# Optimization experiments

Measured on AMD Instinct MI355X. Metric: run time of the kernel, lower is better.

Reference implementation:

```python
import jax, jax.numpy as jnp
import numpy as np

T, D, E, F = 8192, 1024, 8, 3584


def setup_inputs() -> dict:
    key = jax.random.key(0)
    ks = jax.random.split(key, 5)
    scale_in = 1.0 / np.sqrt(D)
    scale_ff = 1.0 / np.sqrt(F)
    return {
        "x": jax.random.normal(ks[0], (T, D), dtype=jnp.float32),
        "w1": jax.random.normal(ks[1], (E, F, D), dtype=jnp.float32) * scale_in,
        "w3": jax.random.normal(ks[2], (E, F, D), dtype=jnp.float32) * scale_in,
        "w2": jax.random.normal(ks[3], (E, D, F), dtype=jnp.float32) * scale_ff,
        "router_logits": jax.random.normal(ks[4], (T, E), dtype=jnp.float32),
        "top_k": 2,
    }


def reference(x, w1, w3, w2, router_logits, top_k):
    # Routing: softmax over experts, keep top-k, renormalize (Mixtral, normalize=True)
    probs = jax.nn.softmax(router_logits, axis=-1)            # [T, E]
    top_vals, top_idx = jax.lax.top_k(probs, top_k)           # [T, k]
    top_vals = top_vals / jnp.sum(top_vals, axis=-1, keepdims=True)
    tokens = jnp.arange(x.shape[0])[:, None]
    weights = jnp.zeros_like(probs).at[tokens, top_idx].set(top_vals)  # [T, E]

    gate = jnp.einsum('td,efd->tef', x, w1)                   # [T, E, F]
    up = jnp.einsum('td,efd->tef', x, w3)                     # [T, E, F]
    h = jax.nn.silu(gate) * up                                # [T, E, F]
    out = jnp.einsum('te,tef,edf->td', weights, h, w2)        # [T, D]
    return out
```

## Files before the change

kernel.cpp:

```cpp
#include <hip/hip_runtime.h>
#include <cstdint>

#define T_TOK 8192
#define D_DIM 1024
#define E_EXP 8
#define F_DIM 3584
#define NROW  (2 * T_TOK)
#define PROWS_PAD 18432
#define MAXTILES 72
#define MAXBANDS 18
#define G1_GRID (MAXBANDS * 112)
#define W2_ELEMS ((long)E_EXP * D_DIM * F_DIM)
#define W2_CVT_BLOCKS ((int)(W2_ELEMS / (512 * 8)))
#define W13_ELEMS ((long)E_EXP * F_DIM * D_DIM)
#define GATH_BLOCKS (PROWS_PAD * 128 / 256)
#define W13_BLOCKS ((int)(W13_ELEMS / 8 / 256))

typedef __attribute__((ext_vector_type(8))) __bf16 bf16x8;
typedef __attribute__((ext_vector_type(4))) float f32x4;

__device__ __forceinline__ void gload16(const void* g, void* l) {
    __builtin_amdgcn_global_load_lds(
        (const __attribute__((address_space(1))) void*)(g),
        (__attribute__((address_space(3))) void*)(l),
        16, 0, 0);
}

__device__ __forceinline__ void cvt8(const float* __restrict__ in, __bf16* __restrict__ out, long i) {
    const float4 f0 = *(const float4*)(in + i);
    const float4 f1 = *(const float4*)(in + i + 4);
    bf16x8 o;
    o[0] = (__bf16)f0.x; o[1] = (__bf16)f0.y; o[2] = (__bf16)f0.z; o[3] = (__bf16)f0.w;
    o[4] = (__bf16)f1.x; o[5] = (__bf16)f1.y; o[6] = (__bf16)f1.z; o[7] = (__bf16)f1.w;
    *(bf16x8*)(out + i) = o;
}

__global__ void cvt_kernel(const float* __restrict__ in, __bf16* __restrict__ out, long n) {
    long i = ((long)blockIdx.x * blockDim.x + threadIdx.x) * 8;
    if (i >= n) return;
    cvt8(in, out, i);
}

__global__ void prep_kernel(const float* __restrict__ x, const int* __restrict__ tokOf,
                            __bf16* __restrict__ xg,
                            const float* __restrict__ w1, __bf16* __restrict__ w1b,
                            const float* __restrict__ w3, __bf16* __restrict__ w3b) {
    const int b = blockIdx.x;
    if (b < GATH_BLOCKS) {
        const int idx = b * 256 + threadIdx.x;
        const int pr = idx >> 7;
        const int j = (idx & 127) * 8;
        const int tk = tokOf[pr];
        bf16x8 o = {};
        if (tk >= 0) {
            const float4 f0 = *(const float4*)(x + (long)tk * D_DIM + j);
            const float4 f1 = *(const float4*)(x + (long)tk * D_DIM + j + 4);
            o[0] = (__bf16)f0.x; o[1] = (__bf16)f0.y; o[2] = (__bf16)f0.z; o[3] = (__bf16)f0.w;
            o[4] = (__bf16)f1.x; o[5] = (__bf16)f1.y; o[6] = (__bf16)f1.z; o[7] = (__bf16)f1.w;
        }
        *(bf16x8*)(xg + (long)pr * D_DIM + j) = o;
    } else if (b < GATH_BLOCKS + W13_BLOCKS) {
        const long i = ((long)(b - GATH_BLOCKS) * 256 + threadIdx.x) * 8;
        if (i < W13_ELEMS) cvt8(w1, w1b, i);
    } else {
        const long i = ((long)(b - GATH_BLOCKS - W13_BLOCKS) * 256 + threadIdx.x) * 8;
        if (i < W13_ELEMS) cvt8(w3, w3b, i);
    }
}

__global__ void route_kernel(const float* __restrict__ rl, int* cnt,
                             int* __restrict__ eidx, float* __restrict__ ewgt) {
    int t = blockIdx.x * blockDim.x + threadIdx.x;
    if (t >= T_TOK) return;
    float l[8];
#pragma unroll
    for (int e = 0; e < 8; ++e) l[e] = rl[t * 8 + e];
    int i0 = 0; float v0 = l[0];
    int i1 = -1; float v1 = -1e30f;
#pragma unroll
    for (int e = 1; e < 8; ++e) {
        if (l[e] > v0) { v1 = v0; i1 = i0; v0 = l[e]; i0 = e; }
        else if (l[e] > v1) { v1 = l[e]; i1 = e; }
    }
    float wsec = 1.f / (1.f + __expf(v0 - v1));
    eidx[2 * t] = i0; eidx[2 * t + 1] = i1;
    ewgt[2 * t] = 1.f - wsec; ewgt[2 * t + 1] = wsec;
    atomicAdd(&cnt[i0], 1); atomicAdd(&cnt[i1], 1);
}

__global__ void scan_kernel(const int* __restrict__ cnt, int* __restrict__ pofs) {
    if (threadIdx.x == 0) {
        int a = 0;
        for (int e = 0; e < E_EXP; ++e) { pofs[e] = a; a += (cnt[e] + 255) & ~255; }
        pofs[E_EXP] = a;
    }
}

__global__ void tiles_kernel(const int* __restrict__ pofs, int* __restrict__ tile_e,
                             int* __restrict__ tile_r0, int* __restrict__ meta) {
    if (threadIdx.x == 0) {
        int n = 0;
        for (int e = 0; e < E_EXP; ++e)
            for (int r = pofs[e]; r < pofs[e + 1]; r += 256) {
                tile_e[n] = e; tile_r0[n] = r; ++n;
            }
        meta[0] = n;
    }
}

__global__ void assign_kernel(const int* __restrict__ eidx, const int* __restrict__ pofs,
                              int* cnt2, int* __restrict__ tokOf, int* __restrict__ rowOf) {
    int t = blockIdx.x * blockDim.x + threadIdx.x;
    if (t >= T_TOK) return;
#pragma unroll
    for (int s = 0; s < 2; ++s) {
        int e = eidx[2 * t + s];
        int pos = atomicAdd(&cnt2[e], 1);
        int prow = pofs[e] + pos;
        tokOf[prow] = t;
        rowOf[2 * t + s] = prow;
    }
}

__device__ __forceinline__ int chunk_row(int c) { return ((c >> 7) << 4) | ((c >> 2) & 15); }
__device__ __forceinline__ int chunk_col(int c) {
    return ((c >> 6) & 1) * 32 + (((c & 3) * 8) ^ (((c >> 5) & 1) << 4));
}

template <int NT>
__device__ __forceinline__ void moe_pipeline(
    const __bf16* const (&srcA)[2][2], const __bf16* const (&srcB)[2][2],
    __bf16 (&Ash)[2][2][8192], __bf16 (&Bsh)[2][2][8192],
    int wave, int abase, int wm, int bh, int bsel, f32x4 (&acc)[8][4])
{
    auto stA = [&](int buf, int kt, int h) {
        const long k0 = (long)kt * 64;
        gload16(srcA[h][0] + k0, &Ash[buf][h][(0 * 512 + wave * 64) * 8]);
        gload16(srcA[h][1] + k0, &Ash[buf][h][(1 * 512 + wave * 64) * 8]);
    };
    auto stB = [&](int buf, int kt, int h) {
        const long k0 = (long)kt * 64;
        gload16(srcB[h][0] + k0, &Bsh[buf][h][(0 * 512 + wave * 64) * 8]);
        gload16(srcB[h][1] + k0, &Bsh[buf][h][(1 * 512 + wave * 64) * 8]);
    };

    bf16x8 bfr[4][2];
    bf16x8 afr[4][2];
    bf16x8 afr2[4][2];

#define LD_A4(dst, Ab, h) \
    _Pragma("unroll") for (int j = 0; j < 4; ++j) { \
        dst[j][0] = *(const bf16x8*)((Ab) + ((4*(h)+j) * 2 + 0) * 512); \
        dst[j][1] = *(const bf16x8*)((Ab) + ((4*(h)+j) * 2 + 1) * 512); \
    }

#define LD_B(Bb) \
    _Pragma("unroll") for (int ni = 0; ni < 4; ++ni) { \
        bfr[ni][0] = *(const bf16x8*)((Bb) + ((bsel * 4 + ni) * 2 + 0) * 512); \
        bfr[ni][1] = *(const bf16x8*)((Bb) + ((bsel * 4 + ni) * 2 + 1) * 512); \
    }

#define MFMA_H(h, src) \
    _Pragma("unroll") for (int j = 0; j < 4; ++j) \
        _Pragma("unroll") for (int ni = 0; ni < 4; ++ni) { \
            acc[4*(h)+j][ni] = __builtin_amdgcn_mfma_f32_16x16x32_bf16(src[j][0], bfr[ni][0], acc[4*(h)+j][ni], 0, 0, 0); \
            acc[4*(h)+j][ni] = __builtin_amdgcn_mfma_f32_16x16x32_bf16(src[j][1], bfr[ni][1], acc[4*(h)+j][ni], 0, 0, 0); \
        }

#define PH_OPEN() \
    __builtin_amdgcn_sched_barrier(0); \
    __builtin_amdgcn_s_barrier(); \
    asm volatile("s_waitcnt lgkmcnt(0)" ::: "memory"); \
    __builtin_amdgcn_sched_barrier(0); \
    __builtin_amdgcn_s_setprio(1);

#define PH_CLOSE() \
    __builtin_amdgcn_s_setprio(0); \
    __builtin_amdgcn_sched_barrier(0); \
    __builtin_amdgcn_s_barrier(); \
    __builtin_amdgcn_sched_barrier(0);

#define PH_CLOSE_G(lastf) \
    __builtin_amdgcn_s_setprio(0); \
    __builtin_amdgcn_sched_barrier(0); \
    if (lastf) { asm volatile("s_waitcnt vmcnt(0)" ::: "memory"); } \
    else       { asm volatile("s_waitcnt vmcnt(4)" ::: "memory"); } \
    __builtin_amdgcn_s_barrier(); \
    __builtin_amdgcn_sched_barrier(0);

    stA(0, 0, 0); stA(0, 0, 1); stB(0, 0, 0); stB(0, 0, 1);
    stB(1, 1, 0); stB(1, 1, 1);
    asm volatile("s_waitcnt vmcnt(4)" ::: "memory");
    __builtin_amdgcn_s_barrier();

    const __bf16* AbE = &Ash[0][wm][abase];
    const __bf16* BbE = &Bsh[0][bh][abase];
    const __bf16* AbO = &Ash[1][wm][abase];
    const __bf16* BbO = &Bsh[1][bh][abase];

    for (int it = 0; it < NT / 2; ++it) {
        const int kv = 2 * it + 1;
        const bool last = (it == NT / 2 - 1);
        LD_A4(afr, AbE, 0) LD_B(BbE)
        stA(1, kv, 0); stA(1, kv, 1);
        PH_OPEN()
        MFMA_H(0, afr)
        LD_A4(afr2, AbE, 1)
        PH_CLOSE()
        if (!last) { stB(0, kv + 1, 0); stB(0, kv + 1, 1); }
        PH_OPEN()
        MFMA_H(1, afr2)
        PH_CLOSE_G(last)
        LD_A4(afr, AbO, 0) LD_B(BbO)
        if (!last) { stA(0, kv + 1, 0); stA(0, kv + 1, 1); }
        PH_OPEN()
        MFMA_H(0, afr)
        LD_A4(afr2, AbO, 1)
        PH_CLOSE()
        if (!last) { stB(1, kv + 2, 0); stB(1, kv + 2, 1); }
        PH_OPEN()
        MFMA_H(1, afr2)
        PH_CLOSE_G(last)
    }
#undef LD_A4
#undef LD_B
#undef MFMA_H
#undef PH_OPEN
#undef PH_CLOSE
#undef PH_CLOSE_G
}

__global__ __launch_bounds__(512, 1)
void gemm1_kernel(const __bf16* __restrict__ xg,
                  const __bf16* __restrict__ w1b,
                  const __bf16* __restrict__ w3b,
                  const int* __restrict__ tile_e,
                  const int* __restrict__ tile_r0,
                  const int* __restrict__ meta,
                  __bf16* __restrict__ h,
                  const float* __restrict__ w2src,
                  __bf16* __restrict__ w2dst) {
    const int bid = blockIdx.x;
    if (bid >= G1_GRID) {
        const long i = ((long)(bid - G1_GRID) * 512 + threadIdx.x) * 8;
        if (i < W2_ELEMS) cvt8(w2src, w2dst, i);
        return;
    }
    const int count = meta[0];
    const int bands = (count + 3) >> 2;
    const int live = bands * 112;
    if (bid >= live) return;
    const int w = (bid & 7) * (live >> 3) + (bid >> 3);
    const int q28 = w / 28, r = w % 28;
    const int tile = (q28 >> 2) * 4 + r / 7;
    const int nt = (q28 & 3) * 7 + r % 7;
    if (tile >= count) return;
    const int e = tile_e[tile];
    const int row0 = tile_r0[tile];

    __shared__ __align__(16) __bf16 Ash[2][2][8192];
    __shared__ __align__(16) __bf16 Bsh[2][2][8192];

    const int tid = threadIdx.x;
    const int wave = tid >> 6, lane = tid & 63;
    const int wm = wave >> 2, wn = wave & 3;
    const int fr = lane & 15, fg = lane >> 4;

    const __bf16* srcA[2][2];
    const __bf16* srcB[2][2];
#pragma unroll
    for (int half = 0; half < 2; ++half)
#pragma unroll
        for (int j = 0; j < 2; ++j) {
            const int c = tid + j * 512;
            srcA[half][j] = xg + (long)(row0 + half * 128 + chunk_row(c)) * D_DIM + chunk_col(c);
            const int rb = half * 128 + chunk_row(c);
            const int blk = rb >> 4;
            const int f = nt * 128 + (blk >> 1) * 16 + (rb & 15);
            srcB[half][j] = ((blk & 1) ? w3b : w1b) + ((long)e * F_DIM + f) * D_DIM + chunk_col(c);
        }

    const int abase = fr * 32 + ((fg * 8) ^ ((fr & 8) << 1));
    f32x4 acc[8][4] = {};

    moe_pipeline<16>(srcA, srcB, Ash, Bsh, wave, abase, wm, wn >> 1, wn & 1, acc);

#pragma unroll
    for (int mi = 0; mi < 8; ++mi) {
#pragma unroll
        for (int reg = 0; reg < 4; ++reg) {
            const int lm = wm * 128 + mi * 16 + fg * 4 + reg;
            const long hrow = (long)(row0 + lm) * F_DIM;
#pragma unroll
            for (int b = 0; b < 2; ++b) {
                const float g = acc[mi][2 * b][reg];
                const float u = acc[mi][2 * b + 1][reg];
                const float s = g / (1.f + __expf(-g));
                h[hrow + nt * 128 + (wn * 2 + b) * 16 + fr] = (__bf16)(s * u);
            }
        }
    }
}

__global__ __launch_bounds__(512, 1)
void gemm2_kernel(const __bf16* __restrict__ hb,
                  const __bf16* __restrict__ w2b,
                  const int* __restrict__ tile_e,
                  const int* __restrict__ tile_r0,
                  const int* __restrict__ meta,
                  __bf16* __restrict__ o2p) {
    const int count = meta[0];
    const int bands = (count + 3) >> 2;
    const int live = bands * 32;
    const int bid = blockIdx.x;
    if (bid >= live) return;
    const int w = (bid & 7) * (live >> 3) + (bid >> 3);
    const int band = w >> 5, s = w & 31;
    const int tile = band * 4 + (s >> 3);
    const int nt = s & 3, ks = (s >> 2) & 1;
    if (tile >= count) return;
    const int e = tile_e[tile];
    const int row0 = tile_r0[tile];

    __shared__ __align__(16) __bf16 Ash[2][2][8192];
    __shared__ __align__(16) __bf16 Bsh[2][2][8192];

    const int tid = threadIdx.x;
    const int wave = tid >> 6, lane = tid & 63;
    const int wm = wave >> 2, wn = wave & 3;
    const int fr = lane & 15, fg = lane >> 4;
    const int kofs = ks * (F_DIM / 2);

    const __bf16* srcA[2][2];
    const __bf16* srcB[2][2];
#pragma unroll
    for (int half = 0; half < 2; ++half)
#pragma unroll
        for (int j = 0; j < 2; ++j) {
            const int c = tid + j * 512;
            srcA[half][j] = hb + (long)(row0 + half * 128 + chunk_row(c)) * F_DIM + kofs + chunk_col(c);
            const int rb = half * 128 + chunk_row(c);
            srcB[half][j] = w2b + ((long)e * D_DIM + nt * 256 + rb) * F_DIM + kofs + chunk_col(c);
        }

    const int abase = fr * 32 + ((fg * 8) ^ ((fr & 8) << 1));
    f32x4 acc[8][4] = {};

    moe_pipeline<28>(srcA, srcB, Ash, Bsh, wave, abase, wm, wn >> 1, wn & 1, acc);

    __bf16* ps = o2p + (long)ks * PROWS_PAD * D_DIM;
#pragma unroll
    for (int mi = 0; mi < 8; ++mi) {
#pragma unroll
        for (int reg = 0; reg < 4; ++reg) {
            const int lm = wm * 128 + mi * 16 + fg * 4 + reg;
            const long obase = (long)(row0 + lm) * D_DIM + nt * 256 + wn * 64 + fr;
#pragma unroll
            for (int ni = 0; ni < 4; ++ni)
                ps[obase + ni * 16] = (__bf16)acc[mi][ni][reg];
        }
    }
}

__global__ void combine_kernel(const __bf16* __restrict__ o2p, const int* __restrict__ rowOf,
                               const float* __restrict__ ewgt, float* __restrict__ out) {
    const int idx = blockIdx.x * blockDim.x + threadIdx.x;
    const int t = idx >> 7;
    const int j = (idx & 127) * 8;
    const long r0 = rowOf[2 * t], r1 = rowOf[2 * t + 1];
    const float w0 = ewgt[2 * t], w1 = ewgt[2 * t + 1];
    float r[8] = {0, 0, 0, 0, 0, 0, 0, 0};
#pragma unroll
    for (int s = 0; s < 2; ++s) {
        const bf16x8 a = *(const bf16x8*)(o2p + ((long)s * PROWS_PAD + r0) * D_DIM + j);
        const bf16x8 b = *(const bf16x8*)(o2p + ((long)s * PROWS_PAD + r1) * D_DIM + j);
#pragma unroll
        for (int q = 0; q < 8; ++q) r[q] += w0 * (float)a[q] + w1 * (float)b[q];
    }
    float4* ob = (float4*)(out + (long)t * D_DIM + j);
    ob[0] = make_float4(r[0], r[1], r[2], r[3]);
    ob[1] = make_float4(r[4], r[5], r[6], r[7]);
}

extern "C" void kernel_launch(void* const* d_in, const int* in_sizes, int n_in,
                              void* d_out, int out_size, void* d_ws, size_t ws_size,
                              hipStream_t stream) {
    const float* x  = (const float*)d_in[0];
    const float* w1 = (const float*)d_in[1];
    const float* w3 = (const float*)d_in[2];
    const float* w2 = (const float*)d_in[3];
    const float* rl = (const float*)d_in[4];
    float* out = (float*)d_out;

    char* ws = (char*)d_ws;
    size_t off = 0;
    auto alloc = [&](size_t bytes) {
        void* p = ws + off;
        off += (bytes + 255) & ~(size_t)255;
        return p;
    };
    __bf16* xg   = (__bf16*)alloc((size_t)PROWS_PAD * D_DIM * 2);
    __bf16* w1b  = (__bf16*)alloc((size_t)E_EXP * F_DIM * D_DIM * 2);
    __bf16* w3b  = (__bf16*)alloc((size_t)E_EXP * F_DIM * D_DIM * 2);
    __bf16* hbuf = (__bf16*)alloc((size_t)PROWS_PAD * F_DIM * 2);
    int*   tokOf = (int*)alloc(PROWS_PAD * 4);
    int*   rowOf = (int*)alloc(NROW * 4);
    int*   eidx  = (int*)alloc(NROW * 4);
    float* ewgt  = (float*)alloc(NROW * 4);
    int*   cnt1  = (int*)alloc(64);
    int*   cnt2  = (int*)alloc(64);
    int*   pofs  = (int*)alloc(64);
    int*   tileE = (int*)alloc(MAXTILES * 4 + 64);
    int*   tileR = (int*)alloc(MAXTILES * 4 + 64);
    int*   meta  = (int*)alloc(64);

    const size_t W2B_BYTES = (size_t)W2_ELEMS * 2;
    const size_t front = off;
    const bool fused = (ws_size >= front + W2B_BYTES);
    __bf16* w2b;
    __bf16* o2p;
    if (fused) {
        w2b = (__bf16*)alloc(W2B_BYTES);
        o2p = (__bf16*)ws;
    } else {
        w2b = (__bf16*)ws;
        o2p = (__bf16*)(ws + W2B_BYTES);
    }

    hipMemsetAsync(cnt1, 0, 64, stream);
    hipMemsetAsync(cnt2, 0, 64, stream);
    hipMemsetAsync(tokOf, 0xFF, PROWS_PAD * 4, stream);

    route_kernel<<<T_TOK / 256, 256, 0, stream>>>(rl, cnt1, eidx, ewgt);
    scan_kernel<<<1, 64, 0, stream>>>(cnt1, pofs);
    tiles_kernel<<<1, 64, 0, stream>>>(pofs, tileE, tileR, meta);
    assign_kernel<<<T_TOK / 256, 256, 0, stream>>>(eidx, pofs, cnt2, tokOf, rowOf);

    prep_kernel<<<GATH_BLOCKS + 2 * W13_BLOCKS, 256, 0, stream>>>(
        x, tokOf, xg, w1, w1b, w3, w3b);

    if (fused) {
        gemm1_kernel<<<G1_GRID + W2_CVT_BLOCKS, 512, 0, stream>>>(
            xg, w1b, w3b, tileE, tileR, meta, hbuf, w2, w2b);
    } else {
        gemm1_kernel<<<G1_GRID, 512, 0, stream>>>(
            xg, w1b, w3b, tileE, tileR, meta, hbuf, w2, w2b);
        cvt_kernel<<<(int)(W2_ELEMS / 8 / 256), 256, 0, stream>>>(w2, w2b, W2_ELEMS);
    }

    gemm2_kernel<<<MAXBANDS * 32, 512, 0, stream>>>(hbuf, w2b, tileE, tileR, meta, o2p);

    combine_kernel<<<T_TOK * (D_DIM / 8) / 256, 256, 0, stream>>>(o2p, rowOf, ewgt, out);
}
```

Before: 650.7 us.

## Switch MoE GEMMs from 16x16x32 to 32x32x16 bf16 MFMA tiles

Replaces the 16x16x32 MFMA fragments with 32x32x16 bf16 MFMA in both expert GEMMs. The LDS chunk layout, the fragment loads and the epilogue index math are reorganised to match the 32x32 output layout. The larger instruction cuts the number of MFMA issues and the LDS fragment reads per FLOP. In exchange, the new LDS layout drops the old XOR swizzle, which risks bank conflicts, and the stores to h and the partial outputs change their access pattern.

```diff
diff --git a/kernel.cpp b/kernel.cpp
--- a/kernel.cpp
+++ b/kernel.cpp
@@ -17,7 +17,7 @@
 #define W13_BLOCKS ((int)(W13_ELEMS / 8 / 256))
 
 typedef __attribute__((ext_vector_type(8))) __bf16 bf16x8;
-typedef __attribute__((ext_vector_type(4))) float f32x4;
+typedef __attribute__((ext_vector_type(16))) float f32x16;
 
 __device__ __forceinline__ void gload16(const void* g, void* l) {
     __builtin_amdgcn_global_load_lds(
@@ -122,16 +122,14 @@
     }
 }
 
-__device__ __forceinline__ int chunk_row(int c) { return ((c >> 7) << 4) | ((c >> 2) & 15); }
-__device__ __forceinline__ int chunk_col(int c) {
-    return ((c >> 6) & 1) * 32 + (((c & 3) * 8) ^ (((c >> 5) & 1) << 4));
-}
+__device__ __forceinline__ int chunk_row32(int c) { return ((c >> 8) << 5) | ((c >> 1) & 31); }
+__device__ __forceinline__ int chunk_col32(int c) { return ((c >> 6) & 3) * 16 + (c & 1) * 8; }
 
 template <int NT>
 __device__ __forceinline__ void moe_pipeline(
     const __bf16* const (&srcA)[2][2], const __bf16* const (&srcB)[2][2],
     __bf16 (&Ash)[2][2][8192], __bf16 (&Bsh)[2][2][8192],
-    int wave, int abase, int wm, int bh, int bsel, f32x4 (&acc)[8][4])
+    int wave, int lane, int wm, int bh, int bsel, f32x16 (&acc)[4][2])
 {
     auto stA = [&](int buf, int kt, int h) {
         const long k0 = (long)kt * 64;
@@ -144,28 +142,27 @@
         gload16(srcB[h][1] + k0, &Bsh[buf][h][(1 * 512 + wave * 64) * 8]);
     };
 
-    bf16x8 bfr[4][2];
-    bf16x8 afr[4][2];
-    bf16x8 afr2[4][2];
-
-#define LD_A4(dst, Ab, h) \
-    _Pragma("unroll") for (int j = 0; j < 4; ++j) { \
-        dst[j][0] = *(const bf16x8*)((Ab) + ((4*(h)+j) * 2 + 0) * 512); \
-        dst[j][1] = *(const bf16x8*)((Ab) + ((4*(h)+j) * 2 + 1) * 512); \
-    }
+    const int lanebase = ((lane & 31) * 2 + (lane >> 5)) * 8;
+
+    bf16x8 bfr[2][4];
+    bf16x8 afr[2][4];
+    bf16x8 afr2[2][4];
+
+#define LD_AH(dst, Ab, hh) \
+    _Pragma("unroll") for (int mi = 0; mi < 2; ++mi) \
+        _Pragma("unroll") for (int s = 0; s < 4; ++s) \
+            dst[mi][s] = *(const bf16x8*)((Ab) + (2*(hh)+mi) * 2048 + s * 512);
 
 #define LD_B(Bb) \
-    _Pragma("unroll") for (int ni = 0; ni < 4; ++ni) { \
-        bfr[ni][0] = *(const bf16x8*)((Bb) + ((bsel * 4 + ni) * 2 + 0) * 512); \
-        bfr[ni][1] = *(const bf16x8*)((Bb) + ((bsel * 4 + ni) * 2 + 1) * 512); \
-    }
-
-#define MFMA_H(h, src) \
-    _Pragma("unroll") for (int j = 0; j < 4; ++j) \
-        _Pragma("unroll") for (int ni = 0; ni < 4; ++ni) { \
-            acc[4*(h)+j][ni] = __builtin_amdgcn_mfma_f32_16x16x32_bf16(src[j][0], bfr[ni][0], acc[4*(h)+j][ni], 0, 0, 0); \
-            acc[4*(h)+j][ni] = __builtin_amdgcn_mfma_f32_16x16x32_bf16(src[j][1], bfr[ni][1], acc[4*(h)+j][ni], 0, 0, 0); \
-        }
+    _Pragma("unroll") for (int ni = 0; ni < 2; ++ni) \
+        _Pragma("unroll") for (int s = 0; s < 4; ++s) \
+            bfr[ni][s] = *(const bf16x8*)((Bb) + (bsel * 2 + ni) * 2048 + s * 512);
+
+#define MFMA_H(hh, src) \
+    _Pragma("unroll") for (int s = 0; s < 4; ++s) \
+        _Pragma("unroll") for (int mi = 0; mi < 2; ++mi) \
+            _Pragma("unroll") for (int ni = 0; ni < 2; ++ni) \
+                acc[2*(hh)+mi][ni] = __builtin_amdgcn_mfma_f32_32x32x16_bf16(src[mi][s], bfr[ni][s], acc[2*(hh)+mi][ni], 0, 0, 0);
 
 #define PH_OPEN() \
     __builtin_amdgcn_sched_barrier(0); \
@@ -193,36 +190,36 @@
     asm volatile("s_waitcnt vmcnt(4)" ::: "memory");
     __builtin_amdgcn_s_barrier();
 
-    const __bf16* AbE = &Ash[0][wm][abase];
-    const __bf16* BbE = &Bsh[0][bh][abase];
-    const __bf16* AbO = &Ash[1][wm][abase];
-    const __bf16* BbO = &Bsh[1][bh][abase];
+    const __bf16* AbE = &Ash[0][wm][lanebase];
+    const __bf16* BbE = &Bsh[0][bh][lanebase];
+    const __bf16* AbO = &Ash[1][wm][lanebase];
+    const __bf16* BbO = &Bsh[1][bh][lanebase];
 
     for (int it = 0; it < NT / 2; ++it) {
         const int kv = 2 * it + 1;
         const bool last = (it == NT / 2 - 1);
-        LD_A4(afr, AbE, 0) LD_B(BbE)
+        LD_AH(afr, AbE, 0) LD_B(BbE)
         stA(1, kv, 0); stA(1, kv, 1);
         PH_OPEN()
         MFMA_H(0, afr)
-        LD_A4(afr2, AbE, 1)
+        LD_AH(afr2, AbE, 1)
         PH_CLOSE()
         if (!last) { stB(0, kv + 1, 0); stB(0, kv + 1, 1); }
         PH_OPEN()
         MFMA_H(1, afr2)
         PH_CLOSE_G(last)
-        LD_A4(afr, AbO, 0) LD_B(BbO)
+        LD_AH(afr, AbO, 0) LD_B(BbO)
         if (!last) { stA(0, kv + 1, 0); stA(0, kv + 1, 1); }
         PH_OPEN()
         MFMA_H(0, afr)
-        LD_A4(afr2, AbO, 1)
+        LD_AH(afr2, AbO, 1)
         PH_CLOSE()
         if (!last) { stB(1, kv + 2, 0); stB(1, kv + 2, 1); }
         PH_OPEN()
         MFMA_H(1, afr2)
         PH_CLOSE_G(last)
     }
-#undef LD_A4
+#undef LD_AH
 #undef LD_B
 #undef MFMA_H
 #undef PH_OPEN
@@ -264,7 +261,7 @@
     const int tid = threadIdx.x;
     const int wave = tid >> 6, lane = tid & 63;
     const int wm = wave >> 2, wn = wave & 3;
-    const int fr = lane & 15, fg = lane >> 4;
+    const int bh = wn >> 1, bsel = wn & 1;
 
     const __bf16* srcA[2][2];
     const __bf16* srcB[2][2];
@@ -273,31 +270,29 @@
 #pragma unroll
         for (int j = 0; j < 2; ++j) {
             const int c = tid + j * 512;
-            srcA[half][j] = xg + (long)(row0 + half * 128 + chunk_row(c)) * D_DIM + chunk_col(c);
-            const int rb = half * 128 + chunk_row(c);
-            const int blk = rb >> 4;
-            const int f = nt * 128 + (blk >> 1) * 16 + (rb & 15);
-            srcB[half][j] = ((blk & 1) ? w3b : w1b) + ((long)e * F_DIM + f) * D_DIM + chunk_col(c);
+            srcA[half][j] = xg + (long)(row0 + half * 128 + chunk_row32(c)) * D_DIM + chunk_col32(c);
+            const int rb = half * 128 + chunk_row32(c);
+            const int blk = rb >> 5;
+            const int f = nt * 128 + (blk >> 1) * 32 + (rb & 31);
+            srcB[half][j] = ((blk & 1) ? w3b : w1b) + ((long)e * F_DIM + f) * D_DIM + chunk_col32(c);
         }
 
-    const int abase = fr * 32 + ((fg * 8) ^ ((fr & 8) << 1));
-    f32x4 acc[8][4] = {};
-
-    moe_pipeline<16>(srcA, srcB, Ash, Bsh, wave, abase, wm, wn >> 1, wn & 1, acc);
-
-#pragma unroll
-    for (int mi = 0; mi < 8; ++mi) {
-#pragma unroll
-        for (int reg = 0; reg < 4; ++reg) {
-            const int lm = wm * 128 + mi * 16 + fg * 4 + reg;
-            const long hrow = (long)(row0 + lm) * F_DIM;
-#pragma unroll
-            for (int b = 0; b < 2; ++b) {
-                const float g = acc[mi][2 * b][reg];
-                const float u = acc[mi][2 * b + 1][reg];
-                const float s = g / (1.f + __expf(-g));
-                h[hrow + nt * 128 + (wn * 2 + b) * 16 + fr] = (__bf16)(s * u);
-            }
+    f32x16 acc[4][2] = {};
+
+    moe_pipeline<16>(srcA, srcB, Ash, Bsh, wave, lane, wm, bh, bsel, acc);
+
+    const int ccol = lane & 31;
+    const int rb4 = 4 * (lane >> 5);
+    const int fcol = nt * 128 + (bh * 2 + bsel) * 32 + ccol;
+#pragma unroll
+    for (int mi = 0; mi < 4; ++mi) {
+#pragma unroll
+        for (int rg = 0; rg < 16; ++rg) {
+            const int row = wm * 128 + mi * 32 + (rg & 3) + 8 * (rg >> 2) + rb4;
+            const float g = acc[mi][0][rg];
+            const float u = acc[mi][1][rg];
+            const float s = g / (1.f + __expf(-g));
+            h[(long)(row0 + row) * F_DIM + fcol] = (__bf16)(s * u);
         }
     }
 }
@@ -328,7 +323,7 @@
     const int tid = threadIdx.x;
     const int wave = tid >> 6, lane = tid & 63;
     const int wm = wave >> 2, wn = wave & 3;
-    const int fr = lane & 15, fg = lane >> 4;
+    const int bh = wn >> 1, bsel = wn & 1;
     const int kofs = ks * (F_DIM / 2);
 
     const __bf16* srcA[2][2];
@@ -338,26 +333,28 @@
 #pragma unroll
         for (int j = 0; j < 2; ++j) {
             const int c = tid + j * 512;
-            srcA[half][j] = hb + (long)(row0 + half * 128 + chunk_row(c)) * F_DIM + kofs + chunk_col(c);
-            const int rb = half * 128 + chunk_row(c);
-            srcB[half][j] = w2b + ((long)e * D_DIM + nt * 256 + rb) * F_DIM + kofs + chunk_col(c);
+            srcA[half][j] = hb + (long)(row0 + half * 128 + chunk_row32(c)) * F_DIM + kofs + chunk_col32(c);
+            const int rb = half * 128 + chunk_row32(c);
+            srcB[half][j] = w2b + ((long)e * D_DIM + nt * 256 + rb) * F_DIM + kofs + chunk_col32(c);
         }
 
-    const int abase = fr * 32 + ((fg * 8) ^ ((fr & 8) << 1));
-    f32x4 acc[8][4] = {};
-
-    moe_pipeline<28>(srcA, srcB, Ash, Bsh, wave, abase, wm, wn >> 1, wn & 1, acc);
+    f32x16 acc[4][2] = {};
+
+    moe_pipeline<28>(srcA, srcB, Ash, Bsh, wave, lane, wm, bh, bsel, acc);
 
     __bf16* ps = o2p + (long)ks * PROWS_PAD * D_DIM;
-#pragma unroll
-    for (int mi = 0; mi < 8; ++mi) {
-#pragma unroll
-        for (int reg = 0; reg < 4; ++reg) {
-            const int lm = wm * 128 + mi * 16 + fg * 4 + reg;
-            const long obase = (long)(row0 + lm) * D_DIM + nt * 256 + wn * 64 + fr;
-#pragma unroll
-            for (int ni = 0; ni < 4; ++ni)
-                ps[obase + ni * 16] = (__bf16)acc[mi][ni][reg];
+    const int ccol = lane & 31;
+    const int rb4 = 4 * (lane >> 5);
+#pragma unroll
+    for (int mi = 0; mi < 4; ++mi) {
+#pragma unroll
+        for (int ni = 0; ni < 2; ++ni) {
+            const int d = nt * 256 + bh * 128 + (bsel * 2 + ni) * 32 + ccol;
+#pragma unroll
+            for (int rg = 0; rg < 16; ++rg) {
+                const int row = wm * 128 + mi * 32 + (rg & 3) + 8 * (rg >> 2) + rb4;
+                ps[(long)(row0 + row) * D_DIM + d] = (__bf16)acc[mi][ni][rg];
+            }
         }
     }
 }
```

Result: slower. 703.3 us (+8.1%).
